# Kernel tuning notes

Hardware: AMD Instinct MI355X
Metric: run time of the kernel (lower is better)

## Reference

```python
import jax, jax.numpy as jnp
import numpy as np

E, D, H, T = 16, 1024, 4096, 8192  # num_expert, d_model, d_hidden (4h), total tokens


def setup_inputs() -> dict:
    key = jax.random.key(0)
    k0, k1, k2, k3, k4 = jax.random.split(key, 5)
    inp = jax.random.normal(k0, (T, D), dtype=jnp.float32)
    # FMoELinear init: kaiming-uniform-like, bound = 1/sqrt(fan_in)
    s1 = 1.0 / np.sqrt(D)
    s2 = 1.0 / np.sqrt(H)
    w1 = jax.random.uniform(k1, (E, H, D), jnp.float32, -s1, s1)  # htoh4 weight [E, out, in]
    b1 = jax.random.uniform(k2, (E, H), jnp.float32, -s1, s1)
    w2 = jax.random.uniform(k3, (E, D, H), jnp.float32, -s2, s2)  # h4toh weight
    b2 = jax.random.uniform(k4, (E, D), jnp.float32, -s2, s2)
    fwd_expert_count = jnp.full((E,), T // E, dtype=jnp.int32)  # tokens per expert (sums to T)
    return dict(inp=inp, w1=w1, b1=b1, w2=w2, b2=b2, fwd_expert_count=fwd_expert_count)


def reference(inp, w1, b1, w2, b2, fwd_expert_count):
    # Grouped GEMM: tokens are sorted by expert; segment e gets expert e's FFN.
    counts = np.asarray(fwd_expert_count)          # static per-expert row counts
    offs = np.concatenate([[0], np.cumsum(counts)])
    outs = []
    for e in range(counts.shape[0]):               # loop over fixed small expert set
        seg = inp[offs[e]:offs[e + 1]]             # [n_e, D]
        h = seg @ w1[e].T + b1[e]                  # htoh4: [n_e, H]
        h = jax.nn.gelu(h, approximate=False)      # torch F.gelu default (exact)
        outs.append(h @ w2[e].T + b2[e])           # h4toh: [n_e, D]
    return jnp.concatenate(outs, axis=0)           # [T, D]
```

## Files before the change

### kernel.cpp

```cpp
#include <hip/hip_runtime.h>
#include <hip/hip_bf16.h>

typedef float f32x4 __attribute__((ext_vector_type(4)));
typedef __bf16 bf16x8 __attribute__((ext_vector_type(8)));
typedef unsigned short u16;
typedef unsigned short u16x4 __attribute__((ext_vector_type(4)));
typedef unsigned short u16x8 __attribute__((ext_vector_type(8)));

__device__ __forceinline__ u16 f2bf(float f) {
  __bf16 h = (__bf16)f;
  return __builtin_bit_cast(u16, h);
}

#define G1_BM 256
#define G1_BN 256
#define G1_BK 32
#define G1_NT 512

__global__ __launch_bounds__(G1_NT, 2)
void ffn_gemm1(const float* __restrict__ Af, const float* __restrict__ Bw,
               const float* __restrict__ bias, u16* __restrict__ Out,
               const int* __restrict__ counts, int E, int T, int N, int K)
{
  int mt = blockIdx.y;
  int row0 = 0, cnt = 0, e = 0;
  for (; e < E; ++e) {
    cnt = counts[e];
    int ntl = (cnt + G1_BM - 1) / G1_BM;
    if (mt < ntl) break;
    mt -= ntl; row0 += cnt;
  }
  if (e >= E) return;
  int valid = cnt - mt * G1_BM; if (valid > G1_BM) valid = G1_BM;
  row0 += mt * G1_BM;
  const int n0 = blockIdx.x * G1_BN;
  const float* Be = Bw + (long long)e * N * K;
  const float* be = bias + (long long)e * N;

  __shared__ u16 As[2][G1_BM * G1_BK];
  __shared__ u16 Bs[2][G1_BN * G1_BK];

  const int t = threadIdx.x;
  const int lane = t & 63;
  const int w = t >> 6, wr = w >> 2, wc = w & 3;

  f32x4 acc[8][4];
#pragma unroll
  for (int i = 0; i < 8; ++i)
#pragma unroll
    for (int j = 0; j < 4; ++j) acc[i][j] = (f32x4){0.f, 0.f, 0.f, 0.f};

  const int NKT = K / G1_BK;

  long long offA[4]; int wAo[4];
  long long offB[4]; int wBo[4];
#pragma unroll
  for (int i = 0; i < 4; ++i) {
    int idx = i * G1_NT + t;
    int row = idx >> 3, col4 = idx & 7;
    int gr = row0 + row; if (gr > T - 1) gr = T - 1;
    offA[i] = (long long)gr * K + col4 * 4;
    wAo[i] = row * G1_BK + (((col4 >> 1) ^ (row & 3)) << 3) + ((col4 & 1) << 2);
    offB[i] = (long long)(n0 + row) * K + col4 * 4;
    wBo[i] = wAo[i] - ((row0 + row <= T - 1 ? 0 : 0));
    wBo[i] = row * G1_BK + (((col4 >> 1) ^ (row & 3)) << 3) + ((col4 & 1) << 2);
  }

  const int rl = lane & 15, kgr = lane >> 4;
  int aoff[8], boff[4];
#pragma unroll
  for (int mf = 0; mf < 8; ++mf) {
    int row = wr * 128 + mf * 16 + rl;
    aoff[mf] = row * G1_BK + ((kgr ^ (rl & 3)) << 3);
  }
#pragma unroll
  for (int nf = 0; nf < 4; ++nf) {
    int row = wc * 64 + nf * 16 + rl;
    boff[nf] = row * G1_BK + ((kgr ^ (rl & 3)) << 3);
  }

  f32x4 a4[4], b4[4];

  auto load_g = [&](int kt) {
    const int k0 = kt * G1_BK;
#pragma unroll
    for (int i = 0; i < 4; ++i) a4[i] = *(const f32x4*)(Af + offA[i] + k0);
#pragma unroll
    for (int i = 0; i < 4; ++i) b4[i] = *(const f32x4*)(Be + offB[i] + k0);
  };

  auto store_tile = [&](int buf) {
#pragma unroll
    for (int i = 0; i < 4; ++i) {
      u16x4 pa = { f2bf(a4[i][0]), f2bf(a4[i][1]), f2bf(a4[i][2]), f2bf(a4[i][3]) };
      *(u16x4*)&As[buf][wAo[i]] = pa;
    }
#pragma unroll
    for (int i = 0; i < 4; ++i) {
      u16x4 pb = { f2bf(b4[i][0]), f2bf(b4[i][1]), f2bf(b4[i][2]), f2bf(b4[i][3]) };
      *(u16x4*)&Bs[buf][wBo[i]] = pb;
    }
  };

  load_g(0);
  store_tile(0);
  load_g(1);
  __syncthreads();

#pragma unroll 2
  for (int kt = 0; kt < NKT; ++kt) {
    const int cur = kt & 1;

    bf16x8 bfr[4], af[8];
#pragma unroll
    for (int nf = 0; nf < 4; ++nf)
      bfr[nf] = __builtin_bit_cast(bf16x8, *(const u16x8*)&Bs[cur][boff[nf]]);
#pragma unroll
    for (int mf = 0; mf < 8; ++mf)
      af[mf] = __builtin_bit_cast(bf16x8, *(const u16x8*)&As[cur][aoff[mf]]);

    if (kt + 1 < NKT) store_tile(cur ^ 1);
    if (kt + 2 < NKT) load_g(kt + 2);

    __builtin_amdgcn_s_setprio(1);
#pragma unroll
    for (int mf = 0; mf < 8; ++mf)
#pragma unroll
      for (int nf = 0; nf < 4; ++nf)
        acc[mf][nf] = __builtin_amdgcn_mfma_f32_16x16x32_bf16(af[mf], bfr[nf], acc[mf][nf], 0, 0, 0);
    __builtin_amdgcn_s_setprio(0);

    __syncthreads();
  }

  const int cl = lane & 15, rg = lane >> 4;
#pragma unroll
  for (int nf = 0; nf < 4; ++nf) {
    int gcol = n0 + wc * 64 + nf * 16 + cl;
    float bv = be[gcol];
#pragma unroll
    for (int mf = 0; mf < 8; ++mf) {
#pragma unroll
      for (int r = 0; r < 4; ++r) {
        int lrow = wr * 128 + mf * 16 + rg * 4 + r;
        if (lrow < valid) {
          float v = acc[mf][nf][r] + bv;
          v = 0.5f * v * (1.0f + erff(v * 0.70710678118654752f));
          Out[(long long)(row0 + lrow) * N + gcol] = f2bf(v);
        }
      }
    }
  }
}

#define BM 128
#define BN 128
#define BK 32
#define NT 256

template<bool A_BF16, bool DO_GELU, bool OUT_BF16>
__global__ __launch_bounds__(NT)
void ffn_gemm(const void* __restrict__ Ain, const float* __restrict__ Bw,
              const float* __restrict__ bias, void* __restrict__ Out,
              const int* __restrict__ counts, int E, int T, int N, int K)
{
  int mt = blockIdx.y;
  int row0 = 0, cnt = 0, e = 0;
  for (; e < E; ++e) {
    cnt = counts[e];
    int ntl = (cnt + BM - 1) / BM;
    if (mt < ntl) break;
    mt -= ntl; row0 += cnt;
  }
  if (e >= E) return;
  int valid = cnt - mt * BM; if (valid > BM) valid = BM;
  row0 += mt * BM;
  const int n0 = blockIdx.x * BN;

  const float* Be = Bw + (long long)e * N * K;
  const float* be = bias + (long long)e * N;

  __shared__ u16 As[2][BM][BK];
  __shared__ u16 Bs[2][BN][BK];

  const int t = threadIdx.x;
  const int lane = t & 63;
  const int w = t >> 6, wr = w >> 1, wc = w & 1;

  f32x4 acc[4][4];
#pragma unroll
  for (int i = 0; i < 4; ++i)
#pragma unroll
    for (int j = 0; j < 4; ++j) acc[i][j] = (f32x4){0.f, 0.f, 0.f, 0.f};

  const int NKT = K / BK;

  long long offA[4];
  if constexpr (!A_BF16) {
#pragma unroll
    for (int i = 0; i < 4; ++i) {
      int c = i * NT + t;
      int row = c >> 3, col = (c & 7) << 2;
      int gr = row0 + row; if (gr > T - 1) gr = T - 1;
      offA[i] = (long long)gr * K + col;
    }
  } else {
#pragma unroll
    for (int i = 0; i < 2; ++i) {
      int c = i * NT + t;
      int row = c >> 2, col = (c & 3) << 3;
      int gr = row0 + row; if (gr > T - 1) gr = T - 1;
      offA[i] = (long long)gr * K + col;
    }
  }
  long long offB[4];
#pragma unroll
  for (int i = 0; i < 4; ++i) {
    int c = i * NT + t;
    int row = c >> 3, col = (c & 7) << 2;
    offB[i] = (long long)(n0 + row) * K + col;
  }

  float rA[16]; u16x8 rAu[2]; float rB[16];

  auto load_g = [&](int kt) {
    const int k0 = kt * BK;
    if constexpr (!A_BF16) {
      const float* Af = (const float*)Ain;
#pragma unroll
      for (int i = 0; i < 4; ++i) {
        f32x4 v = *(const f32x4*)(Af + offA[i] + k0);
        rA[i*4+0] = v[0]; rA[i*4+1] = v[1]; rA[i*4+2] = v[2]; rA[i*4+3] = v[3];
      }
    } else {
      const u16* Ab = (const u16*)Ain;
#pragma unroll
      for (int i = 0; i < 2; ++i)
        rAu[i] = *(const u16x8*)(Ab + offA[i] + k0);
    }
#pragma unroll
    for (int i = 0; i < 4; ++i) {
      f32x4 v = *(const f32x4*)(Be + offB[i] + k0);
      rB[i*4+0] = v[0]; rB[i*4+1] = v[1]; rB[i*4+2] = v[2]; rB[i*4+3] = v[3];
    }
  };

  auto store_tile = [&](int buf) {
    if constexpr (!A_BF16) {
#pragma unroll
      for (int i = 0; i < 4; ++i) {
        int c = i * NT + t;
        int row = c >> 3, col = (c & 7) << 2;
        int kg = (col >> 3) ^ ((row >> 1) & 3);
        int off = kg * 8 + ((col >> 2) & 1) * 4;
        u16x4 pk = { f2bf(rA[i*4+0]), f2bf(rA[i*4+1]), f2bf(rA[i*4+2]), f2bf(rA[i*4+3]) };
        *(u16x4*)&As[buf][row][off] = pk;
      }
    } else {
#pragma unroll
      for (int i = 0; i < 2; ++i) {
        int c = i * NT + t;
        int row = c >> 2, col = (c & 3) << 3;
        int kg = (col >> 3) ^ ((row >> 1) & 3);
        *(u16x8*)&As[buf][row][kg * 8] = rAu[i];
      }
    }
#pragma unroll
    for (int i = 0; i < 4; ++i) {
      int c = i * NT + t;
      int row = c >> 3, col = (c & 7) << 2;
      int kg = (col >> 3) ^ ((row >> 1) & 3);
      int off = kg * 8 + ((col >> 2) & 1) * 4;
      u16x4 pk = { f2bf(rB[i*4+0]), f2bf(rB[i*4+1]), f2bf(rB[i*4+2]), f2bf(rB[i*4+3]) };
      *(u16x4*)&Bs[buf][row][off] = pk;
    }
  };

  load_g(0);
  store_tile(0);
  load_g(1);
  __syncthreads();

  for (int kt = 0; kt < NKT; ++kt) {
    const int cur = kt & 1;

    bf16x8 af[4], bfr[4];
    const int rl = lane & 15;
    const int kg = (lane >> 4) ^ ((rl >> 1) & 3);
#pragma unroll
    for (int mf = 0; mf < 4; ++mf)
      af[mf] = __builtin_bit_cast(bf16x8, *(const u16x8*)&As[cur][wr*64 + mf*16 + rl][kg*8]);
#pragma unroll
    for (int nf = 0; nf < 4; ++nf)
      bfr[nf] = __builtin_bit_cast(bf16x8, *(const u16x8*)&Bs[cur][wc*64 + nf*16 + rl][kg*8]);

    if (kt + 1 < NKT) store_tile(cur ^ 1);
    if (kt + 2 < NKT) load_g(kt + 2);

#pragma unroll
    for (int mf = 0; mf < 4; ++mf)
#pragma unroll
      for (int nf = 0; nf < 4; ++nf)
        acc[mf][nf] = __builtin_amdgcn_mfma_f32_16x16x32_bf16(af[mf], bfr[nf], acc[mf][nf], 0, 0, 0);

    if (kt + 1 < NKT) __syncthreads();
  }

  const int cl = lane & 15, rg = lane >> 4;
#pragma unroll
  for (int mf = 0; mf < 4; ++mf) {
#pragma unroll
    for (int nf = 0; nf < 4; ++nf) {
      int gcol = n0 + wc*64 + nf*16 + cl;
      float bv = be[gcol];
#pragma unroll
      for (int r = 0; r < 4; ++r) {
        int lrow = wr*64 + mf*16 + rg*4 + r;
        if (lrow < valid) {
          float v = acc[mf][nf][r] + bv;
          if constexpr (DO_GELU)
            v = 0.5f * v * (1.0f + erff(v * 0.70710678118654752f));
          long long idx = (long long)(row0 + lrow) * N + gcol;
          if constexpr (OUT_BF16) ((u16*)Out)[idx] = f2bf(v);
          else                    ((float*)Out)[idx] = v;
        }
      }
    }
  }
}

extern "C" void kernel_launch(void* const* d_in, const int* in_sizes, int n_in,
                              void* d_out, int out_size, void* d_ws, size_t ws_size,
                              hipStream_t stream) {
  const float* inp = (const float*)d_in[0];
  const float* w1  = (const float*)d_in[1];
  const float* b1  = (const float*)d_in[2];
  const float* w2  = (const float*)d_in[3];
  const float* b2  = (const float*)d_in[4];
  const int* cnts  = (const int*)d_in[5];

  const int E = in_sizes[5];
  const int H = in_sizes[2] / E;
  const int D = in_sizes[4] / E;
  const int T = in_sizes[0] / D;

  u16* hbuf = (u16*)d_ws;

  const int tiles1 = (T + G1_BM - 1) / G1_BM + E;
  dim3 g1(H / G1_BN, tiles1);
  ffn_gemm1<<<g1, dim3(G1_NT), 0, stream>>>(inp, w1, b1, hbuf, cnts, E, T, H, D);

  const int tiles2 = (T + BM - 1) / BM + E;
  dim3 g2(D / BN, tiles2);
  ffn_gemm<true, false, false><<<g2, dim3(NT), 0, stream>>>(
      (const void*)hbuf, w2, b2, d_out, cnts, E, T, D, H);
}
```

Before: 315.3 us.

## Stage GEMM1 tiles via direct global-to-LDS loads in fp32

The first grouped GEMM now copies A and B tiles straight from global memory into LDS with 16-byte global_load_lds instructions, rather than going through registers and converting to bf16 before the LDS store. Tiles are kept as fp32 in LDS with an XOR swizzle, and the bf16 conversion happens when MFMA fragments are read out. The aim is to cut register pressure and the VALU work on the staging path, and to let the copy overlap better with compute. In exchange, LDS use doubles to about 128KB per block, which likely allows only one block per CU despite the launch bound of 2. Each fragment read also repeats the fp32-to-bf16 conversion and moves twice as many LDS bytes.

```diff
diff --git a/kernel.cpp b/kernel.cpp
--- a/kernel.cpp
+++ b/kernel.cpp
@@ -10,6 +10,12 @@
 __device__ __forceinline__ u16 f2bf(float f) {
   __bf16 h = (__bf16)f;
   return __builtin_bit_cast(u16, h);
+}
+
+typedef const __attribute__((address_space(1))) void GAS;
+typedef __attribute__((address_space(3))) void LAS;
+__device__ __forceinline__ void gl_lds16(const void* g, void* l) {
+  __builtin_amdgcn_global_load_lds((GAS*)g, (LAS*)l, 16, 0, 0);
 }
 
 #define G1_BM 256
@@ -37,8 +43,8 @@
   const float* Be = Bw + (long long)e * N * K;
   const float* be = bias + (long long)e * N;
 
-  __shared__ u16 As[2][G1_BM * G1_BK];
-  __shared__ u16 Bs[2][G1_BN * G1_BK];
+  __shared__ float As[2][G1_BM * G1_BK];
+  __shared__ float Bs[2][G1_BN * G1_BK];
 
   const int t = threadIdx.x;
   const int lane = t & 63;
@@ -52,75 +58,62 @@
 
   const int NKT = K / G1_BK;
 
-  long long offA[4]; int wAo[4];
-  long long offB[4]; int wBo[4];
-#pragma unroll
-  for (int i = 0; i < 4; ++i) {
-    int idx = i * G1_NT + t;
-    int row = idx >> 3, col4 = idx & 7;
-    int gr = row0 + row; if (gr > T - 1) gr = T - 1;
-    offA[i] = (long long)gr * K + col4 * 4;
-    wAo[i] = row * G1_BK + (((col4 >> 1) ^ (row & 3)) << 3) + ((col4 & 1) << 2);
-    offB[i] = (long long)(n0 + row) * K + col4 * 4;
-    wBo[i] = wAo[i] - ((row0 + row <= T - 1 ? 0 : 0));
-    wBo[i] = row * G1_BK + (((col4 >> 1) ^ (row & 3)) << 3) + ((col4 & 1) << 2);
-  }
+  const int l8 = lane >> 3, pg = lane & 7;
+  int sA[4], sB[4], ldsOff[4];
+#pragma unroll
+  for (int c = 0; c < 4; ++c) {
+    int r = w * 32 + c * 8 + l8;
+    int g = pg ^ (r & 7);
+    int grA = row0 + r; if (grA > T - 1) grA = T - 1;
+    sA[c] = grA * K + g * 4;
+    sB[c] = (n0 + r) * K + g * 4;
+    ldsOff[c] = (w * 32 + c * 8) * G1_BK;
+  }
+
+  auto stage = [&](int buf, int kt) {
+    const int k0 = kt * G1_BK;
+#pragma unroll
+    for (int c = 0; c < 4; ++c)
+      gl_lds16(Af + sA[c] + k0, &As[buf][ldsOff[c]]);
+#pragma unroll
+    for (int c = 0; c < 4; ++c)
+      gl_lds16(Be + sB[c] + k0, &Bs[buf][ldsOff[c]]);
+  };
 
   const int rl = lane & 15, kgr = lane >> 4;
   int aoff[8], boff[4];
 #pragma unroll
   for (int mf = 0; mf < 8; ++mf) {
-    int row = wr * 128 + mf * 16 + rl;
-    aoff[mf] = row * G1_BK + ((kgr ^ (rl & 3)) << 3);
+    int R = wr * 128 + mf * 16 + rl;
+    aoff[mf] = R * G1_BK + (((2 * kgr) ^ (R & 7)) << 2);
   }
 #pragma unroll
   for (int nf = 0; nf < 4; ++nf) {
-    int row = wc * 64 + nf * 16 + rl;
-    boff[nf] = row * G1_BK + ((kgr ^ (rl & 3)) << 3);
-  }
-
-  f32x4 a4[4], b4[4];
-
-  auto load_g = [&](int kt) {
-    const int k0 = kt * G1_BK;
-#pragma unroll
-    for (int i = 0; i < 4; ++i) a4[i] = *(const f32x4*)(Af + offA[i] + k0);
-#pragma unroll
-    for (int i = 0; i < 4; ++i) b4[i] = *(const f32x4*)(Be + offB[i] + k0);
+    int R = wc * 64 + nf * 16 + rl;
+    boff[nf] = R * G1_BK + (((2 * kgr) ^ (R & 7)) << 2);
+  }
+
+  auto rdfrag = [&](const float* base, int o) -> bf16x8 {
+    f32x4 lo = *(const f32x4*)(base + o);
+    f32x4 hi = *(const f32x4*)(base + (o ^ 4));
+    u16x8 r = { f2bf(lo[0]), f2bf(lo[1]), f2bf(lo[2]), f2bf(lo[3]),
+                f2bf(hi[0]), f2bf(hi[1]), f2bf(hi[2]), f2bf(hi[3]) };
+    return __builtin_bit_cast(bf16x8, r);
   };
 
-  auto store_tile = [&](int buf) {
-#pragma unroll
-    for (int i = 0; i < 4; ++i) {
-      u16x4 pa = { f2bf(a4[i][0]), f2bf(a4[i][1]), f2bf(a4[i][2]), f2bf(a4[i][3]) };
-      *(u16x4*)&As[buf][wAo[i]] = pa;
-    }
-#pragma unroll
-    for (int i = 0; i < 4; ++i) {
-      u16x4 pb = { f2bf(b4[i][0]), f2bf(b4[i][1]), f2bf(b4[i][2]), f2bf(b4[i][3]) };
-      *(u16x4*)&Bs[buf][wBo[i]] = pb;
-    }
-  };
-
-  load_g(0);
-  store_tile(0);
-  load_g(1);
+  stage(0, 0);
   __syncthreads();
 
-#pragma unroll 2
   for (int kt = 0; kt < NKT; ++kt) {
     const int cur = kt & 1;
 
-    bf16x8 bfr[4], af[8];
-#pragma unroll
-    for (int nf = 0; nf < 4; ++nf)
-      bfr[nf] = __builtin_bit_cast(bf16x8, *(const u16x8*)&Bs[cur][boff[nf]]);
-#pragma unroll
-    for (int mf = 0; mf < 8; ++mf)
-      af[mf] = __builtin_bit_cast(bf16x8, *(const u16x8*)&As[cur][aoff[mf]]);
-
-    if (kt + 1 < NKT) store_tile(cur ^ 1);
-    if (kt + 2 < NKT) load_g(kt + 2);
+    if (kt + 1 < NKT) stage(cur ^ 1, kt + 1);
+
+    bf16x8 af[8], bfr[4];
+#pragma unroll
+    for (int nf = 0; nf < 4; ++nf) bfr[nf] = rdfrag(&Bs[cur][0], boff[nf]);
+#pragma unroll
+    for (int mf = 0; mf < 8; ++mf) af[mf] = rdfrag(&As[cur][0], aoff[mf]);
 
     __builtin_amdgcn_s_setprio(1);
 #pragma unroll
```

Result: slower. 357.4 us (+13.4%).
